# Performance work log

Hardware: AMD Instinct MI355X
Metric: run time of the kernel (lower is better)

## Reference

```python
import jax, jax.numpy as jnp
import numpy as np

B, N = 2, 512
P0, P1, P2 = 16, 32, 32
H = 128
IN0 = P0 + 2 * P1
IN1 = P1 + P0 + 2 * P2
IN2 = 2 * (P2 + P1)        # 128 : 2! permutations of (same + expanded arity-1)


def setup_inputs() -> dict:
    key = jax.random.key(0)
    ks = jax.random.split(key, 15)
    g = lambda k, s: jax.random.normal(k, s, dtype=jnp.float32) * 0.05
    return {
        "x0": jax.random.uniform(ks[0], (B, P0), dtype=jnp.float32),
        "x1": jax.random.uniform(ks[1], (B, N, P1), dtype=jnp.float32),
        "x2": jax.random.uniform(ks[2], (B, N, N, P2), dtype=jnp.float32),
        "W1_0": g(ks[3], (IN0, H)), "b1_0": g(ks[4], (H,)),
        "W2_0": g(ks[5], (H, P0)), "b2_0": g(ks[6], (P0,)),
        "W1_1": g(ks[7], (IN1, H)), "b1_1": g(ks[8], (H,)),
        "W2_1": g(ks[9], (H, P1)), "b2_1": g(ks[10], (P1,)),
        "W1_2": g(ks[11], (IN2, H)), "b1_2": g(ks[12], (H,)),
        "W2_2": g(ks[13], (H, P2)), "b2_2": g(ks[14], (P2,)),
    }


def _mlp(x, W1, b1, W2, b2):
    # _InferenceMLP with hidden layer and apply_sigmoid=True:
    # Linear -> Sigmoid -> Linear -> Sigmoid, applied pointwise over object tuples.
    return jax.nn.sigmoid(jax.nn.sigmoid(x @ W1 + b1) @ W2 + b2)


def reference(x0, x1, x2, W1_0, b1_0, W2_0, b2_0,
              W1_1, b1_1, W2_1, b2_1, W1_2, b1_2, W2_2, b2_2):
    n = x1.shape[1]
    # exclude_self mask for reducing arity-2 -> arity-1: zero out diagonal (i==j)
    m = (1.0 - jnp.eye(n, dtype=x2.dtype))[None, :, :, None]  # [1,N,N,1]
    rmax2 = jnp.max(x2 * m, axis=-2)                  # [B,N,P2] exists
    rmin2 = jnp.min(x2 * m + (1.0 - m), axis=-2)      # [B,N,P2] forall (masked -> 1)
    # arity-1 reduce mask is all-ones (no repeated indices possible)
    rmax1 = jnp.max(x1, axis=-2)                      # [B,P1]
    rmin1 = jnp.min(x1, axis=-2)                      # [B,P1]

    # arity 0: same + reduced(arity 1)
    in0 = jnp.concatenate([x0, rmax1, rmin1], axis=-1)            # [B,IN0]
    out0 = _mlp(in0, W1_0, b1_0, W2_0, b2_0)                      # [B,P0]

    # arity 1: same + expanded(arity 0) + reduced(arity 2)
    exp0 = jnp.broadcast_to(x0[:, None, :], (x0.shape[0], n, x0.shape[1]))
    in1 = jnp.concatenate([x1, exp0, rmax2, rmin2], axis=-1)      # [B,N,IN1]
    out1 = _mlp(in1, W1_1, b1_1, W2_1, b2_1)                      # [B,N,P1]

    # arity 2: same + expanded(arity 1), then concat over the 2! axis permutations
    exp1 = jnp.broadcast_to(x1[:, :, None, :], x2.shape[:3] + (x1.shape[-1],))
    cat2 = jnp.concatenate([x2, exp1], axis=-1)                   # [B,N,N,P2+P1]
    in2 = jnp.concatenate([cat2, jnp.transpose(cat2, (0, 2, 1, 3))], axis=-1)  # [B,N,N,IN2]
    out2 = _mlp(in2, W1_2, b1_2, W2_2, b2_2)                      # [B,N,N,P2]

    return (out0, out1, out2)
```

## Files before the change

### kernel.cpp

```cpp
#include <hip/hip_runtime.h>
#include <hip/hip_bf16.h>

#define BB 2
#define NN 512
#define P0 16
#define P1 32
#define P2 32
#define HH 128

typedef __attribute__((ext_vector_type(8))) short bf16x8;
typedef __attribute__((ext_vector_type(4))) float f32x4;
typedef __attribute__((ext_vector_type(4))) unsigned u32x4;

__device__ __forceinline__ unsigned pkbf(float lo, float hi) {
  __hip_bfloat162 h = __float22bfloat162_rn(float2{lo, hi});
  unsigned r;
  __builtin_memcpy(&r, &h, 4);
  return r;
}

__device__ __forceinline__ float sigm(float x) {
  return __builtin_amdgcn_rcpf(1.0f + __expf(-x));
}

__device__ __forceinline__ bf16x8 pack2(f32x4 a, f32x4 b) {
  u32x4 u;
  u[0] = pkbf(a[0], a[1]);
  u[1] = pkbf(a[2], a[3]);
  u[2] = pkbf(b[0], b[1]);
  u[3] = pkbf(b[2], b[3]);
  return __builtin_bit_cast(bf16x8, u);
}

__global__ __launch_bounds__(256) void k_arity2(
    const float* __restrict__ x0, const float* __restrict__ x1,
    const float* __restrict__ x2,
    const float* __restrict__ W1, const float* __restrict__ b1,
    const float* __restrict__ W2, const float* __restrict__ b2,
    const float* __restrict__ W1_1, const float* __restrict__ b1_1,
    const float* __restrict__ W2_1, const float* __restrict__ b2_1,
    float* __restrict__ out1, float* __restrict__ out2) {
  __shared__ __align__(16) short lw[32 * 64 * 8];
  __shared__ float pm[4][32], pn[4][32];
  __shared__ float in1[112], in2[128];
  __shared__ float hid1[HH], hid2[HH];

  const int tid = threadIdx.x;
  const int bid = blockIdx.x;
  const int b = bid >> 9;
  const int i = bid & 511;

  for (int c = tid; c < 2048; c += 256) {
    const int l = c & 63, th = (c >> 6) & 7, s = c >> 9;
    const int fm = l & 15, fb = l >> 4;
    const int h = 16 * th + fm;
    float v[8];
#pragma unroll
    for (int e = 0; e < 8; ++e) {
      const int k = 32 * s + 4 * fb + (e & 3) + 16 * (e >> 2);
      v[e] = W1[k * HH + h];
    }
    unsigned* dst = (unsigned*)&lw[c * 8];
#pragma unroll
    for (int t = 0; t < 4; ++t) dst[t] = pkbf(v[2 * t], v[2 * t + 1]);
  }

  const int lane = tid & 63;
  const int wv = tid >> 6;
  const int m = lane & 15, bq = lane >> 4;

  bf16x8 w2f[2][4];
#pragma unroll
  for (int pt = 0; pt < 2; ++pt) {
#pragma unroll
    for (int s = 0; s < 4; ++s) {
      const int p = 16 * pt + m;
      float v[8];
#pragma unroll
      for (int e = 0; e < 8; ++e) {
        const int h = 32 * s + 4 * bq + (e & 3) + 16 * (e >> 2);
        v[e] = W2[h * P2 + p];
      }
      u32x4 u;
#pragma unroll
      for (int t = 0; t < 4; ++t) u[t] = pkbf(v[2 * t], v[2 * t + 1]);
      w2f[pt][s] = __builtin_bit_cast(bf16x8, u);
    }
  }

  f32x4 bias1[8];
#pragma unroll
  for (int th = 0; th < 8; ++th)
#pragma unroll
    for (int r = 0; r < 4; ++r) bias1[th][r] = b1[16 * th + 4 * bq + r];
  f32x4 bias2[2];
#pragma unroll
  for (int pt = 0; pt < 2; ++pt)
#pragma unroll
    for (int r = 0; r < 4; ++r) bias2[pt][r] = b2[16 * pt + 4 * bq + r];

  const float* x1bi = x1 + ((size_t)b * NN + i) * P1;
  const bf16x8 f1 = pack2(*(const f32x4*)(x1bi + 4 * bq),
                          *(const f32x4*)(x1bi + 16 + 4 * bq));

  __syncthreads();

  const bf16x8* wl = (const bf16x8*)lw;
  const size_t rowI = (size_t)b * NN + i;

  f32x4 pmx0 = {0.f, 0.f, 0.f, 0.f}, pmx1 = {0.f, 0.f, 0.f, 0.f};
  f32x4 pmn0 = {1.f, 1.f, 1.f, 1.f}, pmn1 = {1.f, 1.f, 1.f, 1.f};

#pragma unroll
  for (int it = 0; it < 4; ++it) {
    const int j = (i + 1 + it * 64 + wv * 16 + m) & 511;
    const int j2 = (j + 256) & 511;

    const float* p0 = x2 + (rowI * NN + j) * P2;
    const float* p2 = x2 + (((size_t)b * NN + j) * NN + i) * P2;
    const float* p3 = x1 + ((size_t)b * NN + j) * P1;
    const float* p4 = x2 + (rowI * NN + j2) * P2;
    const f32x4 c0a = *(const f32x4*)(p0 + 4 * bq), c0b = *(const f32x4*)(p0 + 16 + 4 * bq);
    const f32x4 c2a = *(const f32x4*)(p2 + 4 * bq), c2b = *(const f32x4*)(p2 + 16 + 4 * bq);
    const f32x4 c3a = *(const f32x4*)(p3 + 4 * bq), c3b = *(const f32x4*)(p3 + 16 + 4 * bq);
    const f32x4 c4a = *(const f32x4*)(p4 + 4 * bq), c4b = *(const f32x4*)(p4 + 16 + 4 * bq);

    {
      const bool dg = (j2 == i);
#pragma unroll
      for (int r = 0; r < 4; ++r) {
        pmx0[r] = fmaxf(pmx0[r], fmaxf(c0a[r], dg ? 0.0f : c4a[r]));
        pmx1[r] = fmaxf(pmx1[r], fmaxf(c0b[r], dg ? 0.0f : c4b[r]));
        pmn0[r] = fminf(pmn0[r], fminf(c0a[r], dg ? 1.0f : c4a[r]));
        pmn1[r] = fminf(pmn1[r], fminf(c0b[r], dg ? 1.0f : c4b[r]));
      }
    }

    const bf16x8 f0 = pack2(c0a, c0b);
    const bf16x8 f2 = pack2(c2a, c2b);
    const bf16x8 f3 = pack2(c3a, c3b);

    {
      f32x4 acc[8];
#pragma unroll
      for (int th = 0; th < 8; ++th)
        acc[th] = __builtin_amdgcn_mfma_f32_16x16x32_bf16(wl[(0 + th) * 64 + lane], f0, bias1[th], 0, 0, 0);
#pragma unroll
      for (int th = 0; th < 8; ++th)
        acc[th] = __builtin_amdgcn_mfma_f32_16x16x32_bf16(wl[(8 + th) * 64 + lane], f1, acc[th], 0, 0, 0);
#pragma unroll
      for (int th = 0; th < 8; ++th)
        acc[th] = __builtin_amdgcn_mfma_f32_16x16x32_bf16(wl[(16 + th) * 64 + lane], f2, acc[th], 0, 0, 0);
#pragma unroll
      for (int th = 0; th < 8; ++th)
        acc[th] = __builtin_amdgcn_mfma_f32_16x16x32_bf16(wl[(24 + th) * 64 + lane], f3, acc[th], 0, 0, 0);

      f32x4 acc2[2];
#pragma unroll
      for (int pt = 0; pt < 2; ++pt) acc2[pt] = bias2[pt];
#pragma unroll
      for (int s = 0; s < 4; ++s) {
        float sv[8];
#pragma unroll
        for (int e = 0; e < 4; ++e) {
          sv[e] = sigm(acc[2 * s][e]);
          sv[4 + e] = sigm(acc[2 * s + 1][e]);
        }
        u32x4 u;
#pragma unroll
        for (int t = 0; t < 4; ++t) u[t] = pkbf(sv[2 * t], sv[2 * t + 1]);
        const bf16x8 bf = __builtin_bit_cast(bf16x8, u);
#pragma unroll
        for (int pt = 0; pt < 2; ++pt)
          acc2[pt] = __builtin_amdgcn_mfma_f32_16x16x32_bf16(w2f[pt][s], bf, acc2[pt], 0, 0, 0);
      }

      float* op = out2 + (rowI * NN + j) * P2;
#pragma unroll
      for (int pt = 0; pt < 2; ++pt) {
        f32x4 o;
#pragma unroll
        for (int r = 0; r < 4; ++r) o[r] = sigm(acc2[pt][r]);
        *(f32x4*)(op + 16 * pt + 4 * bq) = o;
      }
    }

    {
      f32x4 acc[8];
#pragma unroll
      for (int th = 0; th < 8; ++th)
        acc[th] = __builtin_amdgcn_mfma_f32_16x16x32_bf16(wl[(0 + th) * 64 + lane], f2, bias1[th], 0, 0, 0);
#pragma unroll
      for (int th = 0; th < 8; ++th)
        acc[th] = __builtin_amdgcn_mfma_f32_16x16x32_bf16(wl[(8 + th) * 64 + lane], f3, acc[th], 0, 0, 0);
#pragma unroll
      for (int th = 0; th < 8; ++th)
        acc[th] = __builtin_amdgcn_mfma_f32_16x16x32_bf16(wl[(16 + th) * 64 + lane], f0, acc[th], 0, 0, 0);
#pragma unroll
      for (int th = 0; th < 8; ++th)
        acc[th] = __builtin_amdgcn_mfma_f32_16x16x32_bf16(wl[(24 + th) * 64 + lane], f1, acc[th], 0, 0, 0);

      f32x4 acc2[2];
#pragma unroll
      for (int pt = 0; pt < 2; ++pt) acc2[pt] = bias2[pt];
#pragma unroll
      for (int s = 0; s < 4; ++s) {
        float sv[8];
#pragma unroll
        for (int e = 0; e < 4; ++e) {
          sv[e] = sigm(acc[2 * s][e]);
          sv[4 + e] = sigm(acc[2 * s + 1][e]);
        }
        u32x4 u;
#pragma unroll
        for (int t = 0; t < 4; ++t) u[t] = pkbf(sv[2 * t], sv[2 * t + 1]);
        const bf16x8 bf = __builtin_bit_cast(bf16x8, u);
#pragma unroll
        for (int pt = 0; pt < 2; ++pt)
          acc2[pt] = __builtin_amdgcn_mfma_f32_16x16x32_bf16(w2f[pt][s], bf, acc2[pt], 0, 0, 0);
      }

      float* op = out2 + (((size_t)b * NN + j) * NN + i) * P2;
#pragma unroll
      for (int pt = 0; pt < 2; ++pt) {
        f32x4 o;
#pragma unroll
        for (int r = 0; r < 4; ++r) o[r] = sigm(acc2[pt][r]);
        *(f32x4*)(op + 16 * pt + 4 * bq) = o;
      }
    }
  }

#pragma unroll
  for (int msk = 1; msk < 16; msk <<= 1) {
#pragma unroll
    for (int r = 0; r < 4; ++r) {
      pmx0[r] = fmaxf(pmx0[r], __shfl_xor(pmx0[r], msk));
      pmx1[r] = fmaxf(pmx1[r], __shfl_xor(pmx1[r], msk));
      pmn0[r] = fminf(pmn0[r], __shfl_xor(pmn0[r], msk));
      pmn1[r] = fminf(pmn1[r], __shfl_xor(pmn1[r], msk));
    }
  }
  if (m == 0) {
#pragma unroll
    for (int r = 0; r < 4; ++r) {
      pm[wv][4 * bq + r] = pmx0[r];  pm[wv][16 + 4 * bq + r] = pmx1[r];
      pn[wv][4 * bq + r] = pmn0[r];  pn[wv][16 + 4 * bq + r] = pmn1[r];
    }
  }
  if (tid >= 64 && tid < 128) {
    const int q = tid - 64;
    const float v = (q < 32) ? x2[(rowI * NN + i) * P2 + q] : x1bi[q - 32];
    in2[q] = v;
    in2[64 + q] = v;
  }
  __syncthreads();

  if (tid < 32) {
    float a = pm[0][tid], c = pn[0][tid];
#pragma unroll
    for (int g = 1; g < 4; ++g) {
      a = fmaxf(a, pm[g][tid]);
      c = fminf(c, pn[g][tid]);
    }
    in1[tid] = x1bi[tid];
    in1[48 + tid] = a;
    in1[80 + tid] = c;
  } else if (tid < 48) {
    in1[tid] = x0[b * P0 + (tid - 32)];
  }
  __syncthreads();

  if (tid < 128) {
    float s = b1_1[tid];
    for (int k = 0; k < 112; ++k) s += in1[k] * W1_1[k * HH + tid];
    hid1[tid] = sigm(s);
  } else {
    const int h = tid - 128;
    float s = b1[h];
    for (int k = 0; k < 128; ++k) s += in2[k] * W1[k * HH + h];
    hid2[h] = sigm(s);
  }
  __syncthreads();

  if (tid < 32) {
    float s = b2_1[tid];
    for (int k = 0; k < 128; ++k) s += hid1[k] * W2_1[k * P1 + tid];
    out1[rowI * P1 + tid] = sigm(s);
  } else if (tid >= 128 && tid < 160) {
    const int p = tid - 128;
    float s = b2[p];
    for (int k = 0; k < 128; ++k) s += hid2[k] * W2[k * P2 + p];
    out2[(rowI * NN + i) * P2 + p] = sigm(s);
  }
}

__global__ __launch_bounds__(256) void k_arity0(
    const float* __restrict__ x0, const float* __restrict__ x1,
    const float* __restrict__ W1, const float* __restrict__ b1,
    const float* __restrict__ W2, const float* __restrict__ b2,
    float* __restrict__ out0) {
  __shared__ float rmx[8][32], rmn[8][32];
  __shared__ float in0[80];
  __shared__ float hid[128];

  const int tid = threadIdx.x;
  const int b = blockIdx.x;
  const int p = tid & 31, jg = tid >> 5;

  float mx = -1e30f, mn = 1e30f;
  for (int j = jg; j < NN; j += 8) {
    const float v = x1[((size_t)b * NN + j) * P1 + p];
    mx = fmaxf(mx, v);
    mn = fminf(mn, v);
  }
  rmx[jg][p] = mx;
  rmn[jg][p] = mn;
  __syncthreads();

  if (tid < 32) {
    float a = rmx[0][tid], c = rmn[0][tid];
#pragma unroll
    for (int g = 1; g < 8; ++g) {
      a = fmaxf(a, rmx[g][tid]);
      c = fminf(c, rmn[g][tid]);
    }
    in0[16 + tid] = a;
    in0[48 + tid] = c;
  } else if (tid < 48) {
    in0[tid - 32] = x0[b * P0 + (tid - 32)];
  }
  __syncthreads();

  if (tid < 128) {
    float s = b1[tid];
    for (int k = 0; k < 80; ++k) s += in0[k] * W1[k * HH + tid];
    hid[tid] = sigm(s);
  }
  __syncthreads();

  if (tid < 16) {
    float s = b2[tid];
    for (int k = 0; k < 128; ++k) s += hid[k] * W2[k * P0 + tid];
    out0[b * P0 + tid] = sigm(s);
  }
}

extern "C" void kernel_launch(void* const* d_in, const int* in_sizes, int n_in,
                              void* d_out, int out_size, void* d_ws, size_t ws_size,
                              hipStream_t stream) {
  const float* x0   = (const float*)d_in[0];
  const float* x1   = (const float*)d_in[1];
  const float* x2   = (const float*)d_in[2];
  const float* W1_0 = (const float*)d_in[3];
  const float* b1_0 = (const float*)d_in[4];
  const float* W2_0 = (const float*)d_in[5];
  const float* b2_0 = (const float*)d_in[6];
  const float* W1_1 = (const float*)d_in[7];
  const float* b1_1 = (const float*)d_in[8];
  const float* W2_1 = (const float*)d_in[9];
  const float* b2_1 = (const float*)d_in[10];
  const float* W1_2 = (const float*)d_in[11];
  const float* b1_2 = (const float*)d_in[12];
  const float* W2_2 = (const float*)d_in[13];
  const float* b2_2 = (const float*)d_in[14];

  float* out0 = (float*)d_out;
  float* out1 = out0 + (size_t)BB * P0;
  float* out2 = out1 + (size_t)BB * NN * P1;

  hipLaunchKernelGGL(k_arity2, dim3(1024), dim3(256), 0, stream,
                     x0, x1, x2, W1_2, b1_2, W2_2, b2_2,
                     W1_1, b1_1, W2_1, b2_1, out1, out2);
  hipLaunchKernelGGL(k_arity0, dim3(2), dim3(256), 0, stream,
                     x0, x1, W1_0, b1_0, W2_0, b2_0, out0);
}
```

Before: 82.25 us.

## Fuse arity-0 kernel into main kernel and raise wave priority around MFMA

Folds the small arity-0 MLP kernel into the main arity-2 kernel as two extra blocks, so only one kernel is launched per call and the serialized second launch goes away. It reuses the existing shared buffers, widening pm/pn to 8 rows. It also wraps the first-layer MFMA chains in s_setprio(1)/s_setprio(0) so waves issuing matrix work get scheduling priority over others on the CU. The extra blocks are tiny, so the added tail cost should be small, but the larger shared arrays could affect occupancy slightly.

```diff
diff --git a/kernel.cpp b/kernel.cpp
--- a/kernel.cpp
+++ b/kernel.cpp
@@ -32,21 +32,68 @@
   return __builtin_bit_cast(bf16x8, u);
 }
 
-__global__ __launch_bounds__(256) void k_arity2(
+__global__ __launch_bounds__(256) void k_fused(
     const float* __restrict__ x0, const float* __restrict__ x1,
     const float* __restrict__ x2,
     const float* __restrict__ W1, const float* __restrict__ b1,
     const float* __restrict__ W2, const float* __restrict__ b2,
     const float* __restrict__ W1_1, const float* __restrict__ b1_1,
     const float* __restrict__ W2_1, const float* __restrict__ b2_1,
-    float* __restrict__ out1, float* __restrict__ out2) {
+    const float* __restrict__ W1_0, const float* __restrict__ b1_0,
+    const float* __restrict__ W2_0, const float* __restrict__ b2_0,
+    float* __restrict__ out0, float* __restrict__ out1,
+    float* __restrict__ out2) {
   __shared__ __align__(16) short lw[32 * 64 * 8];
-  __shared__ float pm[4][32], pn[4][32];
+  __shared__ float pm[8][32], pn[8][32];
   __shared__ float in1[112], in2[128];
   __shared__ float hid1[HH], hid2[HH];
 
   const int tid = threadIdx.x;
   const int bid = blockIdx.x;
+
+  if (bid >= 1024) {
+    const int b = bid - 1024;
+    const int p = tid & 31, jg = tid >> 5;
+
+    float mx = -1e30f, mn = 1e30f;
+    for (int j = jg; j < NN; j += 8) {
+      const float v = x1[((size_t)b * NN + j) * P1 + p];
+      mx = fmaxf(mx, v);
+      mn = fminf(mn, v);
+    }
+    pm[jg][p] = mx;
+    pn[jg][p] = mn;
+    __syncthreads();
+
+    if (tid < 32) {
+      float a = pm[0][tid], c = pn[0][tid];
+#pragma unroll
+      for (int g = 1; g < 8; ++g) {
+        a = fmaxf(a, pm[g][tid]);
+        c = fminf(c, pn[g][tid]);
+      }
+      in1[16 + tid] = a;
+      in1[48 + tid] = c;
+    } else if (tid < 48) {
+      in1[tid - 32] = x0[b * P0 + (tid - 32)];
+    }
+    __syncthreads();
+
+    if (tid < 128) {
+      float s = b1_0[tid];
+      for (int k = 0; k < 80; ++k) s += in1[k] * W1_0[k * HH + tid];
+      hid1[tid] = sigm(s);
+    }
+    __syncthreads();
+
+    if (tid < 16) {
+      float s = b2_0[tid];
+      for (int k = 0; k < 128; ++k) s += hid1[k] * W2_0[k * P0 + tid];
+      out0[b * P0 + tid] = sigm(s);
+    }
+    return;
+  }
+
   const int b = bid >> 9;
   const int i = bid & 511;
 
@@ -142,6 +189,7 @@
 
     {
       f32x4 acc[8];
+      __builtin_amdgcn_s_setprio(1);
 #pragma unroll
       for (int th = 0; th < 8; ++th)
         acc[th] = __builtin_amdgcn_mfma_f32_16x16x32_bf16(wl[(0 + th) * 64 + lane], f0, bias1[th], 0, 0, 0);
@@ -154,6 +202,7 @@
 #pragma unroll
       for (int th = 0; th < 8; ++th)
         acc[th] = __builtin_amdgcn_mfma_f32_16x16x32_bf16(wl[(24 + th) * 64 + lane], f3, acc[th], 0, 0, 0);
+      __builtin_amdgcn_s_setprio(0);
 
       f32x4 acc2[2];
 #pragma unroll
@@ -187,6 +236,7 @@
 
     {
       f32x4 acc[8];
+      __builtin_amdgcn_s_setprio(1);
 #pragma unroll
       for (int th = 0; th < 8; ++th)
         acc[th] = __builtin_amdgcn_mfma_f32_16x16x32_bf16(wl[(0 + th) * 64 + lane], f2, bias1[th], 0, 0, 0);
@@ -199,6 +249,7 @@
 #pragma unroll
       for (int th = 0; th < 8; ++th)
         acc[th] = __builtin_amdgcn_mfma_f32_16x16x32_bf16(wl[(24 + th) * 64 + lane], f1, acc[th], 0, 0, 0);
+      __builtin_amdgcn_s_setprio(0);
 
       f32x4 acc2[2];
 #pragma unroll
@@ -292,57 +343,6 @@
     float s = b2[p];
     for (int k = 0; k < 128; ++k) s += hid2[k] * W2[k * P2 + p];
     out2[(rowI * NN + i) * P2 + p] = sigm(s);
-  }
-}
-
-__global__ __launch_bounds__(256) void k_arity0(
-    const float* __restrict__ x0, const float* __restrict__ x1,
-    const float* __restrict__ W1, const float* __restrict__ b1,
-    const float* __restrict__ W2, const float* __restrict__ b2,
-    float* __restrict__ out0) {
-  __shared__ float rmx[8][32], rmn[8][32];
-  __shared__ float in0[80];
-  __shared__ float hid[128];
-
-  const int tid = threadIdx.x;
-  const int b = blockIdx.x;
-  const int p = tid & 31, jg = tid >> 5;
-
-  float mx = -1e30f, mn = 1e30f;
-  for (int j = jg; j < NN; j += 8) {
-    const float v = x1[((size_t)b * NN + j) * P1 + p];
-    mx = fmaxf(mx, v);
-    mn = fminf(mn, v);
-  }
-  rmx[jg][p] = mx;
-  rmn[jg][p] = mn;
-  __syncthreads();
-
-  if (tid < 32) {
-    float a = rmx[0][tid], c = rmn[0][tid];
-#pragma unroll
-    for (int g = 1; g < 8; ++g) {
-      a = fmaxf(a, rmx[g][tid]);
-      c = fminf(c, rmn[g][tid]);
-    }
-    in0[16 + tid] = a;
-    in0[48 + tid] = c;
-  } else if (tid < 48) {
-    in0[tid - 32] = x0[b * P0 + (tid - 32)];
-  }
-  __syncthreads();
-
-  if (tid < 128) {
-    float s = b1[tid];
-    for (int k = 0; k < 80; ++k) s += in0[k] * W1[k * HH + tid];
-    hid[tid] = sigm(s);
-  }
-  __syncthreads();
-
-  if (tid < 16) {
-    float s = b2[tid];
-    for (int k = 0; k < 128; ++k) s += hid[k] * W2[k * P0 + tid];
-    out0[b * P0 + tid] = sigm(s);
   }
 }
 
@@ -369,9 +369,9 @@
   float* out1 = out0 + (size_t)BB * P0;
   float* out2 = out1 + (size_t)BB * NN * P1;
 
-  hipLaunchKernelGGL(k_arity2, dim3(1024), dim3(256), 0, stream,
+  hipLaunchKernelGGL(k_fused, dim3(1026), dim3(256), 0, stream,
                      x0, x1, x2, W1_2, b1_2, W2_2, b2_2,
-                     W1_1, b1_1, W2_1, b2_1, out1, out2);
-  hipLaunchKernelGGL(k_arity0, dim3(2), dim3(256), 0, stream,
-                     x0, x1, W1_0, b1_0, W2_0, b2_0, out0);
-}
+                     W1_1, b1_1, W2_1, b2_1,
+                     W1_0, b1_0, W2_0, b2_0,
+                     out0, out1, out2);
+}
```

Result: faster. 75.85 us (-7.8%).
